# Kernel tuning notes

Hardware: AMD Instinct MI355X
Metric: run time of the kernel (lower is better)

The kernel has to match this reference:

```python
import jax, jax.numpy as jnp
import numpy as np

N_NODES = 50000
N_EDGES = 800000
D = 128
E_DIM = 32
N_LAYERS = 4
BN_EPS = 1e-5


def setup_inputs() -> dict:
    key = jax.random.key(0)
    ks = jax.random.split(key, 9)
    return {
        "x": jax.random.normal(ks[0], (N_NODES, D), dtype=jnp.float32),
        "edge_attr": jax.random.normal(ks[1], (N_EDGES, E_DIM), dtype=jnp.float32),
        "edge_index": jax.random.randint(ks[2], (2, N_EDGES), 0, N_NODES, dtype=jnp.int64),
        "W_edge": jax.random.normal(ks[3], (N_LAYERS, E_DIM, D), dtype=jnp.float32) * 0.1,
        "b_edge": jnp.zeros((N_LAYERS, D), dtype=jnp.float32),
        "W1": jax.random.normal(ks[4], (N_LAYERS, D, D), dtype=jnp.float32) * 0.1,
        "b1": jnp.zeros((N_LAYERS, D), dtype=jnp.float32),
        "W2": jax.random.normal(ks[5], (N_LAYERS, D, D), dtype=jnp.float32) * 0.1,
        "b2": jnp.zeros((N_LAYERS, D), dtype=jnp.float32),
        "gamma": jnp.ones((N_LAYERS, D), dtype=jnp.float32),
        "beta": jnp.zeros((N_LAYERS, D), dtype=jnp.float32),
    }


def reference(x, edge_attr, edge_index, W_edge, b_edge, W1, b1, W2, b2, gamma, beta):
    src, dst = edge_index[0], edge_index[1]
    n = x.shape[0]
    for i in range(N_LAYERS):
        # GINEConv: message = ReLU(x_src + Lin(edge_attr)); scatter-add to dst
        e = edge_attr @ W_edge[i] + b_edge[i]            # [E, D]
        m = jax.nn.relu(x[src] + e)                      # [E, D]
        agg = jax.ops.segment_sum(m, dst, num_segments=n)  # [N, D]
        h = x + agg                                      # (1+eps)*x, eps=0
        # 2-layer MLP
        h = jax.nn.relu(h @ W1[i] + b1[i]) @ W2[i] + b2[i]
        # BatchNorm (training-mode batch stats, biased var) + ReLU; dropout off
        mean = h.mean(axis=0)
        var = h.var(axis=0)
        h = (h - mean) * jax.lax.rsqrt(var + BN_EPS) * gamma[i] + beta[i]
        x = jax.nn.relu(h)
    return x
```

## Files before the change

kernel.cpp:

```cpp
#include <hip/hip_runtime.h>

#define NN 50000
#define NE 800000
#define DD 128
#define ED 32
#define NL 4
#define BN_EPS 1e-5f
#define SCAN_B 1024
#define NB ((NN + SCAN_B - 1) / SCAN_B)

typedef __attribute__((ext_vector_type(8))) short bf16x8;
typedef __attribute__((ext_vector_type(4))) float f32x4;

__device__ __forceinline__ unsigned short f2bf(float f) {
    unsigned u = __float_as_uint(f);
    u += 0x7fffu + ((u >> 16) & 1u);
    return (unsigned short)(u >> 16);
}
__device__ __forceinline__ float bf2f(unsigned short h) {
    return __uint_as_float((unsigned)h << 16);
}

__global__ __launch_bounds__(256) void hist_kernel(
    const int* __restrict__ edst, int* __restrict__ deg)
{
    const int e = blockIdx.x * 256 + threadIdx.x;
    if (e < NE) atomicAdd(&deg[edst[e]], 1);
}

__global__ __launch_bounds__(256) void scan1_kernel(
    const int* __restrict__ deg, int* __restrict__ rowptr, int* __restrict__ bsum)
{
    __shared__ int sh[256];
    const int t = threadIdx.x, b = blockIdx.x;
    const int base = b * SCAN_B + t * 4;
    int v[4];
#pragma unroll
    for (int j = 0; j < 4; ++j) {
        const int idx = base + j;
        v[j] = (idx < NN) ? deg[idx] : 0;
    }
    sh[t] = v[0] + v[1] + v[2] + v[3];
    __syncthreads();
    for (int off = 1; off < 256; off <<= 1) {
        const int val = (t >= off) ? sh[t - off] : 0;
        __syncthreads();
        sh[t] += val;
        __syncthreads();
    }
    int p = (t == 0) ? 0 : sh[t - 1];
#pragma unroll
    for (int j = 0; j < 4; ++j) {
        const int idx = base + j;
        if (idx < NN) rowptr[idx] = p;
        p += v[j];
    }
    if (t == 255) bsum[b] = sh[255];
}

__global__ void scan2_kernel(int* __restrict__ bsum)
{
    if (threadIdx.x == 0) {
        int acc = 0;
        for (int i = 0; i < NB; ++i) { const int v = bsum[i]; bsum[i] = acc; acc += v; }
    }
}

__global__ __launch_bounds__(256) void scan3_kernel(
    int* __restrict__ rowptr, int* __restrict__ cursor, const int* __restrict__ bsum)
{
    const int idx = blockIdx.x * 256 + threadIdx.x;
    if (idx < NN) {
        const int v = rowptr[idx] + bsum[idx / SCAN_B];
        rowptr[idx] = v;
        cursor[idx] = v;
    }
    if (idx == 0) rowptr[NN] = NE;
}

__global__ __launch_bounds__(256) void scatter_kernel(
    const int* __restrict__ esrc, const int* __restrict__ edst,
    const float* __restrict__ ea, int* __restrict__ cursor,
    int* __restrict__ src_perm, int* __restrict__ dst_perm,
    unsigned short* __restrict__ ea_bf)
{
    const int e = blockIdx.x * 256 + threadIdx.x;
    if (e < NE) {
        const int d = edst[e];
        const int pos = atomicAdd(&cursor[d], 1);
        src_perm[pos] = esrc[e];
        dst_perm[pos] = d;
        const float* er = &ea[(size_t)e * ED];
        unsigned short* ob = &ea_bf[(size_t)pos * ED];
#pragma unroll
        for (int g = 0; g < 8; ++g) {
            const float4 v = *(const float4*)&er[g * 4];
            uint2 p;
            p.x = (unsigned)f2bf(v.x) | ((unsigned)f2bf(v.y) << 16);
            p.y = (unsigned)f2bf(v.z) | ((unsigned)f2bf(v.w) << 16);
            *(uint2*)&ob[g * 4] = p;
        }
    }
}

__global__ __launch_bounds__(256) void wconv_kernel(
    const float* __restrict__ We, unsigned short* __restrict__ wtb)
{
    const int tid = blockIdx.x * 256 + threadIdx.x;
    if (tid < NL * DD * ED) {
        const int l = tid / (DD * ED);
        const int r = tid % (DD * ED);
        const int c = r / ED, k = r % ED;
        wtb[tid] = f2bf(We[(size_t)l * ED * DD + k * DD + c]);
    }
}

__global__ __launch_bounds__(256) void w12conv_kernel(
    const float* __restrict__ W1, const float* __restrict__ W2,
    unsigned short* __restrict__ w1t, unsigned short* __restrict__ w2t)
{
    const int tid = blockIdx.x * 256 + threadIdx.x;
    if (tid < NL * DD * DD) {
        const int l = tid / (DD * DD);
        const int r = tid % (DD * DD);
        const int n = r / DD, k = r % DD;
        const size_t s = (size_t)l * DD * DD + k * DD + n;
        w1t[tid] = f2bf(W1[s]);
        w2t[tid] = f2bf(W2[s]);
    }
}

__global__ __launch_bounds__(256) void edge_mfma_kernel(
    const float* __restrict__ x,
    const unsigned short* __restrict__ eab,
    const int* __restrict__ src_perm,
    const int* __restrict__ dst_perm,
    const unsigned short* __restrict__ wtb,
    const float* __restrict__ be,
    float* __restrict__ agg)
{
    __shared__ unsigned short msgl[256 * 128];
    const int t = threadIdx.x;
    const int wv = t >> 6, ln = t & 63;
    const int l15 = ln & 15, kb = ln >> 4;
    const int e0 = blockIdx.x * 256;

    const int c0 = (2 * wv + 0) * 16 + l15;
    const int c1 = (2 * wv + 1) * 16 + l15;
    const bf16x8 bfr0 = *(const bf16x8*)&wtb[c0 * ED + kb * 8];
    const bf16x8 bfr1 = *(const bf16x8*)&wtb[c1 * ED + kb * 8];

    for (int eg = 0; eg < 16; ++eg) {
        const int edge = eg * 16 + l15;
        const bf16x8 afr = *(const bf16x8*)&eab[(size_t)(e0 + edge) * ED + kb * 8];
        f32x4 z = {0.f, 0.f, 0.f, 0.f};
        const f32x4 d0 = __builtin_amdgcn_mfma_f32_16x16x32_bf16(afr, bfr0, z, 0, 0, 0);
        const f32x4 d1 = __builtin_amdgcn_mfma_f32_16x16x32_bf16(afr, bfr1, z, 0, 0, 0);
#pragma unroll
        for (int j = 0; j < 4; ++j) {
            const int mrow = eg * 16 + kb * 4 + j;
            const int sw = ((mrow >> 2) & 3) << 3;
            const int i0 = (((c0 >> 1) ^ sw) << 1) | (c0 & 1);
            const int i1 = (((c1 >> 1) ^ sw) << 1) | (c1 & 1);
            msgl[mrow * 128 + i0] = f2bf(d0[j]);
            msgl[mrow * 128 + i1] = f2bf(d1[j]);
        }
    }
    __syncthreads();

    const int cbase = e0 + wv * 64;
    const int c2 = ln * 2;
    const float2 bv = *(const float2*)&be[c2];
    float2 acc = {0.f, 0.f};
    int seg_start = 0;
    int dnext = dst_perm[cbase];
    for (int g = 0; g < 8; ++g) {
        const int gb = g * 8;
        int srcs[8], dsts[9];
        dsts[0] = dnext;
#pragma unroll
        for (int q = 1; q < 8; ++q) dsts[q] = dst_perm[cbase + gb + q];
        dsts[8] = (gb + 8 < 64) ? dst_perm[cbase + gb + 8] : -1;
        dnext = dsts[8];
#pragma unroll
        for (int q = 0; q < 8; ++q) srcs[q] = src_perm[cbase + gb + q];
        float2 xv[8];
#pragma unroll
        for (int q = 0; q < 8; ++q)
            xv[q] = *(const float2*)&x[(size_t)srcs[q] * DD + c2];
#pragma unroll
        for (int q = 0; q < 8; ++q) {
            const int i = gb + q;
            const int dw = ln ^ (((i >> 2) & 3) << 3);
            const unsigned mm = *(const unsigned*)&msgl[(wv * 64 + i) * 128 + dw * 2];
            const float mlo = __uint_as_float(mm << 16);
            const float mhi = __uint_as_float(mm & 0xffff0000u);
            acc.x += fmaxf(xv[q].x + mlo + bv.x, 0.f);
            acc.y += fmaxf(xv[q].y + mhi + bv.y, 0.f);
            if (i == 63 || dsts[q + 1] != dsts[q]) {
                float* ap = &agg[(size_t)dsts[q] * DD + c2];
                if (seg_start > 0 && i < 63) {
                    *(float2*)ap = acc;
                } else {
                    unsafeAtomicAdd(ap + 0, acc.x);
                    unsafeAtomicAdd(ap + 1, acc.y);
                }
                acc.x = 0.f; acc.y = 0.f;
                seg_start = i + 1;
            }
        }
    }
}

__global__ __launch_bounds__(256) void mlp_mfma_kernel(
    const float* __restrict__ x, const float* __restrict__ agg,
    float* __restrict__ h2out,
    const unsigned short* __restrict__ w1t,
    const unsigned short* __restrict__ w2t,
    const float* __restrict__ b1, const float* __restrict__ b2,
    float* __restrict__ bns)
{
    __shared__ unsigned short ah[64 * 128];
    __shared__ unsigned short al[64 * 128];
    __shared__ unsigned short bh[64 * 128];
    __shared__ unsigned short bl[64 * 128];
    const int t = threadIdx.x;
    const int wv = t >> 6, ln = t & 63, l15 = ln & 15, kb = ln >> 4;
    const int r0 = blockIdx.x * 64;

#pragma unroll
    for (int p = 0; p < 4; ++p) {
        const int row = p * 16 + (t >> 4);
        const int gc = t & 15;
        const int grow = r0 + row;
        float v[8] = {0.f, 0.f, 0.f, 0.f, 0.f, 0.f, 0.f, 0.f};
        if (grow < NN) {
            const size_t g = (size_t)grow * DD + gc * 8;
            const float4 xa = *(const float4*)&x[g];
            const float4 xc = *(const float4*)&x[g + 4];
            const float4 ga = *(const float4*)&agg[g];
            const float4 gc4 = *(const float4*)&agg[g + 4];
            v[0] = xa.x + ga.x; v[1] = xa.y + ga.y; v[2] = xa.z + ga.z; v[3] = xa.w + ga.w;
            v[4] = xc.x + gc4.x; v[5] = xc.y + gc4.y; v[6] = xc.z + gc4.z; v[7] = xc.w + gc4.w;
        }
        unsigned hiw[4], low[4];
#pragma unroll
        for (int j = 0; j < 4; ++j) {
            const unsigned short h0 = f2bf(v[2 * j]);
            const unsigned short h1 = f2bf(v[2 * j + 1]);
            const unsigned short q0 = f2bf(v[2 * j] - bf2f(h0));
            const unsigned short q1 = f2bf(v[2 * j + 1] - bf2f(h1));
            hiw[j] = (unsigned)h0 | ((unsigned)h1 << 16);
            low[j] = (unsigned)q0 | ((unsigned)q1 << 16);
        }
        const int off = row * 128 + (gc ^ (row & 7)) * 8;
        *(uint4*)&ah[off] = *(uint4*)hiw;
        *(uint4*)&al[off] = *(uint4*)low;
    }

    bf16x8 w1f[2][4];
#pragma unroll
    for (int nt = 0; nt < 2; ++nt) {
        const int n = wv * 32 + nt * 16 + l15;
#pragma unroll
        for (int ks = 0; ks < 4; ++ks)
            w1f[nt][ks] = *(const bf16x8*)&w1t[n * DD + ks * 32 + kb * 8];
    }
    const int cA = wv * 32 + l15, cB = wv * 32 + 16 + l15;
    const float b1v[2] = {b1[cA], b1[cB]};
    const float b2v[2] = {b2[cA], b2[cB]};
    __syncthreads();

    f32x4 acc[4][2];
#pragma unroll
    for (int mt = 0; mt < 4; ++mt)
#pragma unroll
        for (int nt = 0; nt < 2; ++nt)
            acc[mt][nt] = (f32x4){0.f, 0.f, 0.f, 0.f};
#pragma unroll
    for (int ks = 0; ks < 4; ++ks) {
#pragma unroll
        for (int mt = 0; mt < 4; ++mt) {
            const int row = mt * 16 + l15;
            const int off = row * 128 + ((ks * 4 + kb) ^ (row & 7)) * 8;
            const bf16x8 afh = *(const bf16x8*)&ah[off];
            const bf16x8 afl = *(const bf16x8*)&al[off];
#pragma unroll
            for (int nt = 0; nt < 2; ++nt) {
                acc[mt][nt] = __builtin_amdgcn_mfma_f32_16x16x32_bf16(afh, w1f[nt][ks], acc[mt][nt], 0, 0, 0);
                acc[mt][nt] = __builtin_amdgcn_mfma_f32_16x16x32_bf16(afl, w1f[nt][ks], acc[mt][nt], 0, 0, 0);
            }
        }
    }

#pragma unroll
    for (int mt = 0; mt < 4; ++mt) {
#pragma unroll
        for (int nt = 0; nt < 2; ++nt) {
            const int col = wv * 32 + nt * 16 + l15;
#pragma unroll
            for (int j = 0; j < 4; ++j) {
                const int row = mt * 16 + kb * 4 + j;
                const float v = fmaxf(acc[mt][nt][j] + b1v[nt], 0.f);
                const unsigned short hi = f2bf(v);
                const int off = row * 128 + ((col >> 3) ^ (row & 7)) * 8 + (col & 7);
                bh[off] = hi;
                bl[off] = f2bf(v - bf2f(hi));
            }
        }
    }

    bf16x8 w2f[2][4];
#pragma unroll
    for (int nt = 0; nt < 2; ++nt) {
        const int n = wv * 32 + nt * 16 + l15;
#pragma unroll
        for (int ks = 0; ks < 4; ++ks)
            w2f[nt][ks] = *(const bf16x8*)&w2t[n * DD + ks * 32 + kb * 8];
    }
    __syncthreads();

#pragma unroll
    for (int mt = 0; mt < 4; ++mt)
#pragma unroll
        for (int nt = 0; nt < 2; ++nt)
            acc[mt][nt] = (f32x4){0.f, 0.f, 0.f, 0.f};
#pragma unroll
    for (int ks = 0; ks < 4; ++ks) {
#pragma unroll
        for (int mt = 0; mt < 4; ++mt) {
            const int row = mt * 16 + l15;
            const int off = row * 128 + ((ks * 4 + kb) ^ (row & 7)) * 8;
            const bf16x8 afh = *(const bf16x8*)&bh[off];
            const bf16x8 afl = *(const bf16x8*)&bl[off];
#pragma unroll
            for (int nt = 0; nt < 2; ++nt) {
                acc[mt][nt] = __builtin_amdgcn_mfma_f32_16x16x32_bf16(afh, w2f[nt][ks], acc[mt][nt], 0, 0, 0);
                acc[mt][nt] = __builtin_amdgcn_mfma_f32_16x16x32_bf16(afl, w2f[nt][ks], acc[mt][nt], 0, 0, 0);
            }
        }
    }

    float ps[2] = {0.f, 0.f}, pq[2] = {0.f, 0.f};
#pragma unroll
    for (int mt = 0; mt < 4; ++mt) {
#pragma unroll
        for (int nt = 0; nt < 2; ++nt) {
            const int col = wv * 32 + nt * 16 + l15;
#pragma unroll
            for (int j = 0; j < 4; ++j) {
                const int row = r0 + mt * 16 + kb * 4 + j;
                const float v = acc[mt][nt][j] + b2v[nt];
                if (row < NN) {
                    h2out[(size_t)row * DD + col] = v;
                    ps[nt] += v;
                    pq[nt] += v * v;
                }
            }
        }
    }
#pragma unroll
    for (int nt = 0; nt < 2; ++nt) {
        ps[nt] += __shfl_xor(ps[nt], 16);
        ps[nt] += __shfl_xor(ps[nt], 32);
        pq[nt] += __shfl_xor(pq[nt], 16);
        pq[nt] += __shfl_xor(pq[nt], 32);
    }
    if (kb == 0) {
#pragma unroll
        for (int nt = 0; nt < 2; ++nt) {
            const int col = wv * 32 + nt * 16 + l15;
            unsafeAtomicAdd(&bns[col], ps[nt]);
            unsafeAtomicAdd(&bns[DD + col], pq[nt]);
        }
    }
}

__global__ __launch_bounds__(256) void bn_apply(
    const float* __restrict__ h2, const float* __restrict__ bns,
    const float* __restrict__ gamma, const float* __restrict__ beta,
    float* __restrict__ xout)
{
    const size_t i = ((size_t)blockIdx.x * 256 + threadIdx.x) * 4;
    if (i >= (size_t)NN * DD) return;
    const int c4 = (int)(i & 127);
    const float4 hv = *(const float4*)&h2[i];
    const float4 sv = *(const float4*)&bns[c4];
    const float4 qv = *(const float4*)&bns[DD + c4];
    const float4 gv = *(const float4*)&gamma[c4];
    const float4 bv = *(const float4*)&beta[c4];
    const float inv_n = 1.f / (float)NN;
    float4 ov;
    {
        const float m = sv.x * inv_n;
        const float var = qv.x * inv_n - m * m;
        ov.x = fmaxf((hv.x - m) * __frsqrt_rn(var + BN_EPS) * gv.x + bv.x, 0.f);
    }
    {
        const float m = sv.y * inv_n;
        const float var = qv.y * inv_n - m * m;
        ov.y = fmaxf((hv.y - m) * __frsqrt_rn(var + BN_EPS) * gv.y + bv.y, 0.f);
    }
    {
        const float m = sv.z * inv_n;
        const float var = qv.z * inv_n - m * m;
        ov.z = fmaxf((hv.z - m) * __frsqrt_rn(var + BN_EPS) * gv.z + bv.z, 0.f);
    }
    {
        const float m = sv.w * inv_n;
        const float var = qv.w * inv_n - m * m;
        ov.w = fmaxf((hv.w - m) * __frsqrt_rn(var + BN_EPS) * gv.w + bv.w, 0.f);
    }
    *(float4*)&xout[i] = ov;
}

extern "C" void kernel_launch(void* const* d_in, const int* in_sizes, int n_in,
                              void* d_out, int out_size, void* d_ws, size_t ws_size,
                              hipStream_t stream) {
    const float* x0    = (const float*)d_in[0];
    const float* ea    = (const float*)d_in[1];
    const int*   eidx  = (const int*)d_in[2];
    const float* We    = (const float*)d_in[3];
    const float* be    = (const float*)d_in[4];
    const float* W1    = (const float*)d_in[5];
    const float* b1    = (const float*)d_in[6];
    const float* W2    = (const float*)d_in[7];
    const float* b2    = (const float*)d_in[8];
    const float* gamma = (const float*)d_in[9];
    const float* beta  = (const float*)d_in[10];
    float* out = (float*)d_out;
    float* ws  = (float*)d_ws;

    float* agg = ws;
    float* xb  = agg + (size_t)NN * DD;
    float* bns = xb + (size_t)NN * DD;
    int* deg      = (int*)(bns + 256);
    int* rowptr   = deg + 50000;
    int* cursor   = rowptr + 50004;
    int* bsum     = cursor + 50000;
    int* src_perm = bsum + 64;
    int* dst_perm = src_perm + NE;
    unsigned short* ea_bf = (unsigned short*)(dst_perm + NE);
    unsigned short* wt_bf = ea_bf + (size_t)NE * ED;
    unsigned short* w1t   = wt_bf + (size_t)NL * DD * ED;
    unsigned short* w2t   = w1t + (size_t)NL * DD * DD;

    const int* esrc = eidx;
    const int* edst = eidx + NE;

    hipMemsetAsync(deg, 0, NN * sizeof(int), stream);
    hist_kernel<<<(NE + 255) / 256, 256, 0, stream>>>(edst, deg);
    scan1_kernel<<<NB, 256, 0, stream>>>(deg, rowptr, bsum);
    scan2_kernel<<<1, 64, 0, stream>>>(bsum);
    scan3_kernel<<<(NN + 255) / 256, 256, 0, stream>>>(rowptr, cursor, bsum);
    scatter_kernel<<<(NE + 255) / 256, 256, 0, stream>>>(
        esrc, edst, ea, cursor, src_perm, dst_perm, ea_bf);
    wconv_kernel<<<(NL * DD * ED + 255) / 256, 256, 0, stream>>>(We, wt_bf);
    w12conv_kernel<<<(NL * DD * DD + 255) / 256, 256, 0, stream>>>(W1, W2, w1t, w2t);

    const float* xcur = x0;
    for (int l = 0; l < NL; ++l) {
        hipMemsetAsync(agg, 0, (size_t)NN * DD * sizeof(float), stream);
        hipMemsetAsync(bns, 0, 2 * DD * sizeof(float), stream);
        edge_mfma_kernel<<<NE / 256, 256, 0, stream>>>(
            xcur, ea_bf, src_perm, dst_perm,
            wt_bf + (size_t)l * DD * ED, be + (size_t)l * DD, agg);
        mlp_mfma_kernel<<<(NN + 63) / 64, 256, 0, stream>>>(
            xcur, agg, agg,
            w1t + (size_t)l * DD * DD, w2t + (size_t)l * DD * DD,
            b1 + (size_t)l * DD, b2 + (size_t)l * DD, bns);
        float* xn = (l == NL - 1) ? out : xb;
        bn_apply<<<(NN * DD / 4 + 255) / 256, 256, 0, stream>>>(
            agg, bns, gamma + (size_t)l * DD, beta + (size_t)l * DD, xn);
        xcur = xn;
    }
}
```

Baseline: 736.5 us.

## Halve edge and MLP block tiles, pack src/dst indices, raise occupancy

Edge kernel now processes 128 edges per block instead of 256, and the MLP kernel 32 rows instead of 64. This cuts shared memory per block and adds a min-blocks launch bound so more blocks can be resident. Source and destination indices are interleaved into one int2 array so each group's indices arrive in wide vector loads rather than separate scalar loads. Shorter segments per wave mean more partial sums hit block boundaries, so more atomic adds and more blocks are needed.

Result: faster. 714.3 us (-3.0%).

```diff
diff --git a/kernel.cpp b/kernel.cpp
--- a/kernel.cpp
+++ b/kernel.cpp
@@ -8,6 +8,8 @@
 #define BN_EPS 1e-5f
 #define SCAN_B 1024
 #define NB ((NN + SCAN_B - 1) / SCAN_B)
+#define EB 128
+#define MR 32
 
 typedef __attribute__((ext_vector_type(8))) short bf16x8;
 typedef __attribute__((ext_vector_type(4))) float f32x4;
@@ -81,15 +83,13 @@
 __global__ __launch_bounds__(256) void scatter_kernel(
     const int* __restrict__ esrc, const int* __restrict__ edst,
     const float* __restrict__ ea, int* __restrict__ cursor,
-    int* __restrict__ src_perm, int* __restrict__ dst_perm,
-    unsigned short* __restrict__ ea_bf)
+    int2* __restrict__ sd_perm, unsigned short* __restrict__ ea_bf)
 {
     const int e = blockIdx.x * 256 + threadIdx.x;
     if (e < NE) {
         const int d = edst[e];
         const int pos = atomicAdd(&cursor[d], 1);
-        src_perm[pos] = esrc[e];
-        dst_perm[pos] = d;
+        sd_perm[pos] = make_int2(esrc[e], d);
         const float* er = &ea[(size_t)e * ED];
         unsigned short* ob = &ea_bf[(size_t)pos * ED];
 #pragma unroll
@@ -130,27 +130,27 @@
     }
 }
 
-__global__ __launch_bounds__(256) void edge_mfma_kernel(
+__global__ __launch_bounds__(256, 5) void edge_mfma_kernel(
     const float* __restrict__ x,
     const unsigned short* __restrict__ eab,
-    const int* __restrict__ src_perm,
-    const int* __restrict__ dst_perm,
+    const int2* __restrict__ sd_perm,
     const unsigned short* __restrict__ wtb,
     const float* __restrict__ be,
     float* __restrict__ agg)
 {
-    __shared__ unsigned short msgl[256 * 128];
+    __shared__ unsigned short msgl[EB * 128];
     const int t = threadIdx.x;
     const int wv = t >> 6, ln = t & 63;
     const int l15 = ln & 15, kb = ln >> 4;
-    const int e0 = blockIdx.x * 256;
+    const int e0 = blockIdx.x * EB;
 
     const int c0 = (2 * wv + 0) * 16 + l15;
     const int c1 = (2 * wv + 1) * 16 + l15;
     const bf16x8 bfr0 = *(const bf16x8*)&wtb[c0 * ED + kb * 8];
     const bf16x8 bfr1 = *(const bf16x8*)&wtb[c1 * ED + kb * 8];
 
-    for (int eg = 0; eg < 16; ++eg) {
+#pragma unroll
+    for (int eg = 0; eg < EB / 16; ++eg) {
         const int edge = eg * 16 + l15;
         const bf16x8 afr = *(const bf16x8*)&eab[(size_t)(e0 + edge) * ED + kb * 8];
         f32x4 z = {0.f, 0.f, 0.f, 0.f};
@@ -168,22 +168,25 @@
     }
     __syncthreads();
 
-    const int cbase = e0 + wv * 64;
+    const int lbase = wv * 32;
+    const int2* sdp = &sd_perm[e0 + lbase];
     const int c2 = ln * 2;
     const float2 bv = *(const float2*)&be[c2];
     float2 acc = {0.f, 0.f};
     int seg_start = 0;
-    int dnext = dst_perm[cbase];
-    for (int g = 0; g < 8; ++g) {
+#pragma unroll 1
+    for (int g = 0; g < 4; ++g) {
         const int gb = g * 8;
-        int srcs[8], dsts[9];
-        dsts[0] = dnext;
-#pragma unroll
-        for (int q = 1; q < 8; ++q) dsts[q] = dst_perm[cbase + gb + q];
-        dsts[8] = (gb + 8 < 64) ? dst_perm[cbase + gb + 8] : -1;
-        dnext = dsts[8];
-#pragma unroll
-        for (int q = 0; q < 8; ++q) srcs[q] = src_perm[cbase + gb + q];
+        int4 pr[4];
+#pragma unroll
+        for (int q = 0; q < 4; ++q)
+            pr[q] = *(const int4*)&sdp[gb + 2 * q];
+        const int srcs[8] = {pr[0].x, pr[0].z, pr[1].x, pr[1].z,
+                             pr[2].x, pr[2].z, pr[3].x, pr[3].z};
+        int dsts[9];
+        dsts[0] = pr[0].y; dsts[1] = pr[0].w; dsts[2] = pr[1].y; dsts[3] = pr[1].w;
+        dsts[4] = pr[2].y; dsts[5] = pr[2].w; dsts[6] = pr[3].y; dsts[7] = pr[3].w;
+        dsts[8] = (gb + 8 < 32) ? sdp[gb + 8].y : -1;
         float2 xv[8];
 #pragma unroll
         for (int q = 0; q < 8; ++q)
@@ -192,14 +195,14 @@
         for (int q = 0; q < 8; ++q) {
             const int i = gb + q;
             const int dw = ln ^ (((i >> 2) & 3) << 3);
-            const unsigned mm = *(const unsigned*)&msgl[(wv * 64 + i) * 128 + dw * 2];
+            const unsigned mm = *(const unsigned*)&msgl[(lbase + i) * 128 + dw * 2];
             const float mlo = __uint_as_float(mm << 16);
             const float mhi = __uint_as_float(mm & 0xffff0000u);
             acc.x += fmaxf(xv[q].x + mlo + bv.x, 0.f);
             acc.y += fmaxf(xv[q].y + mhi + bv.y, 0.f);
-            if (i == 63 || dsts[q + 1] != dsts[q]) {
+            if (i == 31 || dsts[q + 1] != dsts[q]) {
                 float* ap = &agg[(size_t)dsts[q] * DD + c2];
-                if (seg_start > 0 && i < 63) {
+                if (seg_start > 0 && i < 31) {
                     *(float2*)ap = acc;
                 } else {
                     unsafeAtomicAdd(ap + 0, acc.x);
@@ -212,7 +215,7 @@
     }
 }
 
-__global__ __launch_bounds__(256) void mlp_mfma_kernel(
+__global__ __launch_bounds__(256, 5) void mlp_mfma_kernel(
     const float* __restrict__ x, const float* __restrict__ agg,
     float* __restrict__ h2out,
     const unsigned short* __restrict__ w1t,
@@ -220,16 +223,16 @@
     const float* __restrict__ b1, const float* __restrict__ b2,
     float* __restrict__ bns)
 {
-    __shared__ unsigned short ah[64 * 128];
-    __shared__ unsigned short al[64 * 128];
-    __shared__ unsigned short bh[64 * 128];
-    __shared__ unsigned short bl[64 * 128];
+    __shared__ unsigned short ah[MR * 128];
+    __shared__ unsigned short al[MR * 128];
+    __shared__ unsigned short bh[MR * 128];
+    __shared__ unsigned short bl[MR * 128];
     const int t = threadIdx.x;
     const int wv = t >> 6, ln = t & 63, l15 = ln & 15, kb = ln >> 4;
-    const int r0 = blockIdx.x * 64;
-
-#pragma unroll
-    for (int p = 0; p < 4; ++p) {
+    const int r0 = blockIdx.x * MR;
+
+#pragma unroll
+    for (int p = 0; p < 2; ++p) {
         const int row = p * 16 + (t >> 4);
         const int gc = t & 15;
         const int grow = r0 + row;
@@ -271,16 +274,16 @@
     const float b2v[2] = {b2[cA], b2[cB]};
     __syncthreads();
 
-    f32x4 acc[4][2];
-#pragma unroll
-    for (int mt = 0; mt < 4; ++mt)
+    f32x4 acc[2][2];
+#pragma unroll
+    for (int mt = 0; mt < 2; ++mt)
 #pragma unroll
         for (int nt = 0; nt < 2; ++nt)
             acc[mt][nt] = (f32x4){0.f, 0.f, 0.f, 0.f};
 #pragma unroll
     for (int ks = 0; ks < 4; ++ks) {
 #pragma unroll
-        for (int mt = 0; mt < 4; ++mt) {
+        for (int mt = 0; mt < 2; ++mt) {
             const int row = mt * 16 + l15;
             const int off = row * 128 + ((ks * 4 + kb) ^ (row & 7)) * 8;
             const bf16x8 afh = *(const bf16x8*)&ah[off];
@@ -294,7 +297,7 @@
     }
 
 #pragma unroll
-    for (int mt = 0; mt < 4; ++mt) {
+    for (int mt = 0; mt < 2; ++mt) {
 #pragma unroll
         for (int nt = 0; nt < 2; ++nt) {
             const int col = wv * 32 + nt * 16 + l15;
@@ -321,14 +324,14 @@
     __syncthreads();
 
 #pragma unroll
-    for (int mt = 0; mt < 4; ++mt)
+    for (int mt = 0; mt < 2; ++mt)
 #pragma unroll
         for (int nt = 0; nt < 2; ++nt)
             acc[mt][nt] = (f32x4){0.f, 0.f, 0.f, 0.f};
 #pragma unroll
     for (int ks = 0; ks < 4; ++ks) {
 #pragma unroll
-        for (int mt = 0; mt < 4; ++mt) {
+        for (int mt = 0; mt < 2; ++mt) {
             const int row = mt * 16 + l15;
             const int off = row * 128 + ((ks * 4 + kb) ^ (row & 7)) * 8;
             const bf16x8 afh = *(const bf16x8*)&bh[off];
@@ -343,7 +346,7 @@
 
     float ps[2] = {0.f, 0.f}, pq[2] = {0.f, 0.f};
 #pragma unroll
-    for (int mt = 0; mt < 4; ++mt) {
+    for (int mt = 0; mt < 2; ++mt) {
 #pragma unroll
         for (int nt = 0; nt < 2; ++nt) {
             const int col = wv * 32 + nt * 16 + l15;
@@ -438,9 +441,8 @@
     int* rowptr   = deg + 50000;
     int* cursor   = rowptr + 50004;
     int* bsum     = cursor + 50000;
-    int* src_perm = bsum + 64;
-    int* dst_perm = src_perm + NE;
-    unsigned short* ea_bf = (unsigned short*)(dst_perm + NE);
+    int2* sd_perm = (int2*)(bsum + 64);
+    unsigned short* ea_bf = (unsigned short*)(sd_perm + NE);
     unsigned short* wt_bf = ea_bf + (size_t)NE * ED;
     unsigned short* w1t   = wt_bf + (size_t)NL * DD * ED;
     unsigned short* w2t   = w1t + (size_t)NL * DD * DD;
@@ -454,7 +456,7 @@
     scan2_kernel<<<1, 64, 0, stream>>>(bsum);
     scan3_kernel<<<(NN + 255) / 256, 256, 0, stream>>>(rowptr, cursor, bsum);
     scatter_kernel<<<(NE + 255) / 256, 256, 0, stream>>>(
-        esrc, edst, ea, cursor, src_perm, dst_perm, ea_bf);
+        esrc, edst, ea, cursor, sd_perm, ea_bf);
     wconv_kernel<<<(NL * DD * ED + 255) / 256, 256, 0, stream>>>(We, wt_bf);
     w12conv_kernel<<<(NL * DD * DD + 255) / 256, 256, 0, stream>>>(W1, W2, w1t, w2t);
 
@@ -462,10 +464,10 @@
     for (int l = 0; l < NL; ++l) {
         hipMemsetAsync(agg, 0, (size_t)NN * DD * sizeof(float), stream);
         hipMemsetAsync(bns, 0, 2 * DD * sizeof(float), stream);
-        edge_mfma_kernel<<<NE / 256, 256, 0, stream>>>(
-            xcur, ea_bf, src_perm, dst_perm,
+        edge_mfma_kernel<<<NE / EB, 256, 0, stream>>>(
+            xcur, ea_bf, sd_perm,
             wt_bf + (size_t)l * DD * ED, be + (size_t)l * DD, agg);
-        mlp_mfma_kernel<<<(NN + 63) / 64, 256, 0, stream>>>(
+        mlp_mfma_kernel<<<(NN + MR - 1) / MR, 256, 0, stream>>>(
             xcur, agg, agg,
             w1t + (size_t)l * DD * DD, w2t + (size_t)l * DD * DD,
             b1 + (size_t)l * DD, b2 + (size_t)l * DD, bns);
```
